# Kernel tuning notes

Measured on AMD Instinct MI355X. Metric: run time of the kernel, lower is better.

## Reference

```python
import jax, jax.numpy as jnp
import numpy as np

B = 4
C = 256
NUM_LEVELS = 5
REFINE_LEVEL = 2
NUM_POINTS = 9
GRAD_MUL = 0.1
SIZES = [160, 80, 40, 20, 10]


def conv2d(x, w, b=None, pad=0):
    out = jax.lax.conv_general_dilated(
        x, w, (1, 1), [(pad, pad), (pad, pad)],
        dimension_numbers=("NCHW", "OIHW", "NCHW"))
    if b is not None:
        out = out + b[None, :, None, None]
    return out


def nearest_resize(x, oh, ow):
    # torch F.interpolate(mode='nearest'): src index = floor(dst * in/out)
    H, W = x.shape[-2], x.shape[-1]
    iy = (jnp.arange(oh) * H) // oh
    ix = (jnp.arange(ow) * W) // ow
    return jnp.take(jnp.take(x, iy, axis=-2), ix, axis=-1)


def max_pool_to(x, oh, ow):
    # adaptive_max_pool2d with exactly-divisible sizes == strided max pool
    b, c, H, W = x.shape
    kh, kw = H // oh, W // ow
    return x.reshape(b, c, oh, kh, ow, kw).max(axis=(3, 5))


def deform_conv(x, offset, weight):
    # DeformConv v1 (mmcv), stride 1, pad 1, 3x3 kernel, no bias.
    # offset channels interleaved (dy, dx) per kernel point.
    b, c, H, W = x.shape
    K = weight.shape[-2] * weight.shape[-1]  # 9
    dy = offset[:, 0::2]  # (B,K,H,W)
    dx = offset[:, 1::2]
    base = jnp.arange(-1, 2, dtype=x.dtype)
    base_y = jnp.repeat(base, 3)  # (9,)
    base_x = jnp.tile(base, 3)
    py = jnp.arange(H, dtype=x.dtype)[None, None, :, None] + base_y[None, :, None, None] + dy
    px = jnp.arange(W, dtype=x.dtype)[None, None, None, :] + base_x[None, :, None, None] + dx
    y0 = jnp.floor(py)
    x0 = jnp.floor(px)
    xf = x.reshape(b, c, H * W)

    def gather(iy, ix):
        valid = ((iy >= 0) & (iy <= H - 1) & (ix >= 0) & (ix <= W - 1)).astype(x.dtype)
        flat = (jnp.clip(iy, 0, H - 1).astype(jnp.int32) * W
                + jnp.clip(ix, 0, W - 1).astype(jnp.int32)).reshape(b, -1)
        g = jax.vmap(lambda xb, ib: jnp.take(xb, ib, axis=1))(xf, flat)
        return g.reshape(b, c, K, H, W) * valid[:, None]

    wy1 = py - y0
    wx1 = px - x0
    wy0 = 1.0 - wy1
    wx0 = 1.0 - wx1
    val = (gather(y0, x0) * (wy0 * wx0)[:, None]
           + gather(y0, x0 + 1.0) * (wy0 * wx1)[:, None]
           + gather(y0 + 1.0, x0) * (wy1 * wx0)[:, None]
           + gather(y0 + 1.0, x0 + 1.0) * (wy1 * wx1)[:, None])  # (B,C,K,H,W)
    return jnp.einsum("bckhw,ock->bohw", val, weight.reshape(weight.shape[0], c, K))


def setup_inputs() -> dict:
    key = jax.random.key(0)
    ks = jax.random.split(key, 12)
    inp = {}
    for i, s in enumerate(SIZES):
        inp[f"x{i}"] = jax.random.normal(ks[i], (B, C, s, s), jnp.float32)
    inp["w_red1"] = jax.random.normal(ks[5], (NUM_LEVELS, 1, C, 3, 3), jnp.float32) * 0.02
    inp["b_red1"] = jnp.zeros((NUM_LEVELS, 1), jnp.float32)
    inp["w_red2"] = jax.random.normal(ks[6], (NUM_LEVELS, 1, C, 3, 3), jnp.float32) * 0.02
    inp["b_red2"] = jnp.zeros((NUM_LEVELS, 1), jnp.float32)
    inp["w_pts_conv"] = jax.random.normal(ks[7], (C, C, 3, 3), jnp.float32) * 0.02
    inp["b_pts_conv"] = jnp.zeros((C,), jnp.float32)
    inp["w_pts_out"] = jax.random.normal(ks[8], (2 * NUM_POINTS, C, 1, 1), jnp.float32) * 0.01
    inp["b_pts_out"] = jnp.zeros((2 * NUM_POINTS,), jnp.float32)
    inp["w_refine"] = jax.random.normal(ks[9], (C, C, 3, 3), jnp.float32) * 0.01
    return inp


def reference(x0, x1, x2, x3, x4, w_red1, b_red1, w_red2, b_red2,
              w_pts_conv, b_pts_conv, w_pts_out, b_pts_out, w_refine):
    inputs = [x0, x1, x2, x3, x4]
    gh, gw = inputs[REFINE_LEVEL].shape[-2], inputs[REFINE_LEVEL].shape[-1]
    feats = [max_pool_to(xi, gh, gw) if i < REFINE_LEVEL else nearest_resize(xi, gh, gw)
             for i, xi in enumerate(inputs)]
    ori_fe = sum(feats) / len(feats)

    pts = conv2d(jax.nn.relu(conv2d(ori_fe, w_pts_conv, b_pts_conv, pad=1)),
                 w_pts_out, b_pts_out, pad=0)
    pts_gm = (1.0 - GRAD_MUL) * jax.lax.stop_gradient(pts) + GRAD_MUL * pts

    base = jnp.arange(-1, 2, dtype=jnp.float32)
    base_off = jnp.stack([jnp.repeat(base, 3), jnp.tile(base, 3)], axis=1).reshape(-1)
    dcn_offset = pts_gm - base_off[None, :, None, None]

    bsf = jax.nn.relu(deform_conv(ori_fe, dcn_offset, w_refine))

    outs = []
    for i, xi in enumerate(inputs):
        h, w = xi.shape[-2], xi.shape[-1]
        # ConvModule default: conv -> (no norm) -> ReLU; then tanh per forward
        basic = jnp.tanh(jax.nn.relu(conv2d(xi, w_red1[i], b_red1[i], pad=1)))
        com = jnp.tanh(jax.nn.relu(conv2d(xi, w_red2[i], b_red2[i], pad=1)))
        att = nearest_resize(bsf, h, w) * (basic + com)
        outs.append(xi + att)
    return tuple(outs)
```

## Files before the change

kernel.cpp:

```cpp
#include <hip/hip_runtime.h>
#include <hip/hip_bf16.h>
#include <math.h>

constexpr int B_ = 4;
constexpr int C_ = 256;
constexpr int GH = 40, GW = 40, GP = 1600;
constexpr int KDIM = C_ * 9;
constexpr int MT = B_ * GP;

typedef __attribute__((ext_vector_type(8))) short short8b;
typedef __attribute__((ext_vector_type(4))) float f32x4;

__device__ inline ushort f2b(float f) {
    __hip_bfloat16 h = __float2bfloat16(f);
    return *reinterpret_cast<ushort*>(&h);
}
__device__ inline float b2f(ushort u) {
    unsigned v = (unsigned)u << 16;
    return *reinterpret_cast<float*>(&v);
}

__global__ __launch_bounds__(256) void fe_kernel(const float* __restrict__ x0,
                                                 const float* __restrict__ x1,
                                                 const float* __restrict__ x2,
                                                 const float* __restrict__ x3,
                                                 const float* __restrict__ x4,
                                                 float* __restrict__ fe_pm) {
    __shared__ float tile[64][65];
    int pix0 = blockIdx.x * 64;
    int c0 = blockIdx.y * 64;
    int b = blockIdx.z;
    int lx = threadIdx.x & 63;
    int ly = threadIdx.x >> 6;

    int pix = pix0 + lx;
    int h = pix / GW, w = pix - (pix / GW) * GW;
#pragma unroll
    for (int r = 0; r < 64; r += 4) {
        int c = c0 + ly + r;
        size_t bc = (size_t)b * C_ + c;
        const float* p0 = x0 + bc * 25600;
        float m0 = -INFINITY;
#pragma unroll
        for (int dy = 0; dy < 4; ++dy)
#pragma unroll
            for (int dx = 0; dx < 4; ++dx)
                m0 = fmaxf(m0, p0[(4 * h + dy) * 160 + 4 * w + dx]);
        const float* p1 = x1 + bc * 6400;
        float m1 = -INFINITY;
#pragma unroll
        for (int dy = 0; dy < 2; ++dy)
#pragma unroll
            for (int dx = 0; dx < 2; ++dx)
                m1 = fmaxf(m1, p1[(2 * h + dy) * 80 + 2 * w + dx]);
        float v2 = x2[bc * GP + pix];
        float v3 = x3[bc * 400 + (h / 2) * 20 + (w / 2)];
        float v4 = x4[bc * 100 + (h / 4) * 10 + (w / 4)];
        tile[ly + r][lx] = (m0 + m1 + v2 + v3 + v4) * 0.2f;
    }
    __syncthreads();
#pragma unroll
    for (int r = 0; r < 64; r += 4) {
        int p = ly + r;
        fe_pm[((size_t)b * GP + pix0 + p) * C_ + c0 + lx] = tile[lx][p];
    }
}

__global__ void wcvt_kernel(const float* __restrict__ wA, const float* __restrict__ wB,
                            ushort* __restrict__ oA, ushort* __restrict__ oB) {
    const float* w = blockIdx.y ? wB : wA;
    ushort* out = blockIdx.y ? oB : oA;
    int idx = blockIdx.x * 256 + threadIdx.x;
    int o = idx / KDIM;
    int rem = idx - o * KDIM;
    int c = rem / 9, t = rem - c * 9;
    out[(size_t)o * KDIM + t * 256 + c] = f2b(w[idx]);
}

__global__ void im2col_kernel(const float* __restrict__ fe_pm, ushort* __restrict__ A1) {
    int pix = blockIdx.x % GP, b = blockIdx.x / GP;
    int c = threadIdx.x;
    const float* fb = fe_pm + (size_t)b * GP * C_;
    ushort* dst = A1 + (size_t)blockIdx.x * KDIM;
    int h = pix / GW, w = pix - (pix / GW) * GW;
#pragma unroll
    for (int t = 0; t < 9; ++t) {
        int y = h + t / 3 - 1, x = w + t % 3 - 1;
        float v = (y >= 0 && y < GH && x >= 0 && x < GW) ? fb[(size_t)(y * GW + x) * C_ + c]
                                                         : 0.f;
        dst[t * 256 + c] = f2b(v);
    }
}

__global__ void sample_kernel(const float* __restrict__ fe_pm, const float* __restrict__ pts,
                              ushort* __restrict__ S) {
    int pix = blockIdx.x % GP, b = blockIdx.x / GP;
    int c = threadIdx.x;
    const float* fb = fe_pm + (size_t)b * GP * C_;
    const float* pb = pts + (size_t)b * 18 * GP + pix;
    ushort* dst = S + (size_t)blockIdx.x * KDIM;
    int h = pix / GW, w = pix - (pix / GW) * GW;
#pragma unroll
    for (int t = 0; t < 9; ++t) {
        float py = (float)h + pb[(2 * t) * GP];
        float px = (float)w + pb[(2 * t + 1) * GP];
        float y0f = floorf(py), x0f = floorf(px);
        int y0 = (int)y0f, x0 = (int)x0f;
        float wy1 = py - y0f, wx1 = px - x0f;
        float wy0 = 1.f - wy1, wx0 = 1.f - wx1;
        auto tap = [&](int yy, int xx) -> float {
            return (yy >= 0 && yy < GH && xx >= 0 && xx < GW)
                       ? fb[(size_t)(yy * GW + xx) * C_ + c]
                       : 0.f;
        };
        float v = tap(y0, x0) * wy0 * wx0 + tap(y0, x0 + 1) * wy0 * wx1 +
                  tap(y0 + 1, x0) * wy1 * wx0 + tap(y0 + 1, x0 + 1) * wy1 * wx1;
        dst[t * 256 + c] = f2b(v);
    }
}

__global__ __launch_bounds__(256) void mfma_gemm(const ushort* __restrict__ A,
                                                 const ushort* __restrict__ Bw,
                                                 const float* __restrict__ bias,
                                                 float* __restrict__ Cout) {
    __shared__ ushort As[2][64 * 64];
    __shared__ ushort Bs[2][64 * 64];
    int tid = threadIdx.x;
    int lane = tid & 63;
    int wid = tid >> 6;
    int wm = wid >> 1, wn = wid & 1;
    int m0 = blockIdx.x * 64;
    int n0 = blockIdx.y * 64;

    int sr = tid >> 3;
    int ss = tid & 7;
    int wsl = (ss ^ (sr & 7)) * 8;
    const ushort* gA0 = A + (size_t)(m0 + sr) * KDIM + ss * 8;
    const ushort* gA1 = A + (size_t)(m0 + sr + 32) * KDIM + ss * 8;
    const ushort* gB0 = Bw + (size_t)(n0 + sr) * KDIM + ss * 8;
    const ushort* gB1 = Bw + (size_t)(n0 + sr + 32) * KDIM + ss * 8;

    f32x4 acc[2][2];
#pragma unroll
    for (int i = 0; i < 2; ++i)
#pragma unroll
        for (int j = 0; j < 2; ++j) acc[i][j] = (f32x4){0.f, 0.f, 0.f, 0.f};

    short8b xA0, xA1, xB0, xB1;
    short8b yA0, yA1, yB0, yB1;

    auto loadX = [&]() {
        xA0 = *(const short8b*)gA0; xA1 = *(const short8b*)gA1;
        xB0 = *(const short8b*)gB0; xB1 = *(const short8b*)gB1;
        gA0 += 64; gA1 += 64; gB0 += 64; gB1 += 64;
    };
    auto loadY = [&]() {
        yA0 = *(const short8b*)gA0; yA1 = *(const short8b*)gA1;
        yB0 = *(const short8b*)gB0; yB1 = *(const short8b*)gB1;
        gA0 += 64; gA1 += 64; gB0 += 64; gB1 += 64;
    };
    auto writeL = [&](int buf, short8b a0, short8b a1, short8b b0, short8b b1) {
        *(short8b*)(As[buf] + sr * 64 + wsl) = a0;
        *(short8b*)(As[buf] + (sr + 32) * 64 + wsl) = a1;
        *(short8b*)(Bs[buf] + sr * 64 + wsl) = b0;
        *(short8b*)(Bs[buf] + (sr + 32) * 64 + wsl) = b1;
    };
    auto compute = [&](int cur) {
#pragma unroll
        for (int kq = 0; kq < 2; ++kq) {
            int k16 = kq * 4 + (lane >> 4);
            short8b af[2], bfr[2];
#pragma unroll
            for (int i = 0; i < 2; ++i) {
                int rA = wm * 32 + i * 16 + (lane & 15);
                af[i] = *(const short8b*)(As[cur] + rA * 64 + ((k16 ^ (rA & 7)) * 8));
                int rB = wn * 32 + i * 16 + (lane & 15);
                bfr[i] = *(const short8b*)(Bs[cur] + rB * 64 + ((k16 ^ (rB & 7)) * 8));
            }
#pragma unroll
            for (int in = 0; in < 2; ++in)
#pragma unroll
                for (int im = 0; im < 2; ++im)
                    acc[in][im] = __builtin_amdgcn_mfma_f32_16x16x32_bf16(
                        bfr[in], af[im], acc[in][im], 0, 0, 0);
        }
    };

    constexpr int NCH = KDIM / 64;
    loadX();
    loadY();
    writeL(0, xA0, xA1, xB0, xB1);
    __syncthreads();

    for (int kc = 0; kc < NCH; kc += 2) {
        if (kc + 2 < NCH) loadX();
        compute(0);
        writeL(1, yA0, yA1, yB0, yB1);
        __syncthreads();
        if (kc + 3 < NCH) loadY();
        compute(1);
        if (kc + 2 < NCH) writeL(0, xA0, xA1, xB0, xB1);
        __syncthreads();
    }

    int b = m0 / GP;
    int pix0 = m0 - b * GP;
    float* Cb = Cout + (size_t)b * C_ * GP;
#pragma unroll
    for (int in = 0; in < 2; ++in) {
#pragma unroll
        for (int r = 0; r < 4; ++r) {
            int n = n0 + wn * 32 + in * 16 + (lane >> 4) * 4 + r;
            float bv = bias ? bias[n] : 0.f;
#pragma unroll
            for (int im = 0; im < 2; ++im) {
                int m = pix0 + wm * 32 + im * 16 + (lane & 15);
                Cb[(size_t)n * GP + m] = fmaxf(acc[in][im][r] + bv, 0.f);
            }
        }
    }
}

__global__ void pts_kernel(const float* __restrict__ p1, const float* __restrict__ wpo,
                           const float* __restrict__ bpo, float* __restrict__ pts) {
    int idx = blockIdx.x * 256 + threadIdx.x;
    int pix = idx % GP;
    int p = (idx / GP) % 18;
    int b = idx / (GP * 18);
    const float* pb = p1 + (size_t)b * C_ * GP + pix;
    const float* wp = wpo + p * C_;
    float s = bpo[p];
    for (int c = 0; c < C_; ++c) s += pb[(size_t)c * GP] * wp[c];
    pts[idx] = s;
}

__device__ constexpr int L_S[5] = {160, 80, 40, 20, 10};
__device__ constexpr int L_NPX[5] = {102400, 25600, 6400, 1600, 400};
__device__ constexpr int YK_START[5] = {0, 400, 500, 525, 532};
__device__ constexpr int FC_START[5] = {0, 1600, 2000, 2100, 2125};
__device__ constexpr size_t L_YBASE[5] = {0, 7372800, 9216000, 9676800, 9792000};
__device__ constexpr size_t L_OUT[5] = {0, 26214400, 32768000, 34406400, 34816000};

__device__ inline int lvl_of(int bx, const int* start) {
    return (bx >= start[4]) ? 4 : (bx >= start[3]) ? 3 : (bx >= start[2]) ? 2
           : (bx >= start[1]) ? 1 : 0;
}

__global__ __launch_bounds__(256) void yk_all(const float* __restrict__ x0,
                                              const float* __restrict__ x1,
                                              const float* __restrict__ x2,
                                              const float* __restrict__ x3,
                                              const float* __restrict__ x4,
                                              const float* __restrict__ w_red1,
                                              const float* __restrict__ w_red2,
                                              ushort* __restrict__ y_all) {
    int bx = blockIdx.x;
    int lvl = lvl_of(bx, YK_START);
    const float* x = lvl == 0 ? x0 : lvl == 1 ? x1 : lvl == 2 ? x2 : lvl == 3 ? x3 : x4;
    int s = L_S[lvl];
    int npx = L_NPX[lvl];
    int bp = (bx - YK_START[lvl]) * 256 + threadIdx.x;
    int g = blockIdx.y;
    if (bp >= npx) return;
    int ss_ = s * s;
    int b = bp / ss_;
    int p = bp - b * ss_;
    const float* xg = x + ((size_t)b * C_ + g * 64) * ss_ + p;
    const float* w1g = w_red1 + (size_t)lvl * KDIM + g * 64 * 9;
    const float* w2g = w_red2 + (size_t)lvl * KDIM + g * 64 * 9;
    float a1[9] = {}, a2[9] = {};
#pragma unroll 4
    for (int ci = 0; ci < 64; ++ci) {
        float v = xg[(size_t)ci * ss_];
#pragma unroll
        for (int t = 0; t < 9; ++t) {
            a1[t] += w1g[ci * 9 + t] * v;
            a2[t] += w2g[ci * 9 + t] * v;
        }
    }
    ushort* yb = y_all + L_YBASE[lvl] + bp;
#pragma unroll
    for (int t = 0; t < 9; ++t) {
        yb[(size_t)(g * 18 + t) * npx] = f2b(a1[t]);
        yb[(size_t)(g * 18 + 9 + t) * npx] = f2b(a2[t]);
    }
}

__global__ __launch_bounds__(256) void fincomb_all(const float* __restrict__ x0,
                                                   const float* __restrict__ x1,
                                                   const float* __restrict__ x2,
                                                   const float* __restrict__ x3,
                                                   const float* __restrict__ x4,
                                                   const ushort* __restrict__ y_all,
                                                   const float* __restrict__ b_red1,
                                                   const float* __restrict__ b_red2,
                                                   const float* __restrict__ bsf,
                                                   float* __restrict__ out) {
    __shared__ float red[2][4][64];
    __shared__ float amap_s[64];
    int bx = blockIdx.x;
    int lvl = lvl_of(bx, FC_START);
    const float* x = lvl == 0 ? x0 : lvl == 1 ? x1 : lvl == 2 ? x2 : lvl == 3 ? x3 : x4;
    int s = L_S[lvl];
    int npx = L_NPX[lvl];
    const ushort* y = y_all + L_YBASE[lvl];
    float* out_l = out + L_OUT[lvl];
    int lane = threadIdx.x & 63;
    int grp = threadIdx.x >> 6;
    int pix_g = (bx - FC_START[lvl]) * 64 + lane;
    bool valid = pix_g < npx;
    int pg = valid ? pix_g : 0;
    int ss_ = s * s;
    int b = pg / ss_;
    int pix = pg - b * ss_;
    int h = pix / s, w = pix - h * s;
    const ushort* yg = y + (size_t)grp * 18 * npx;
    float s1 = 0.f, s2 = 0.f;
#pragma unroll
    for (int t = 0; t < 9; ++t) {
        int dy = t / 3 - 1, dx = t % 3 - 1;
        int hy = h + dy, wx = w + dx;
        if (hy >= 0 && hy < s && wx >= 0 && wx < s) {
            int qq = pg + dy * s + dx;
            s1 += b2f(yg[(size_t)t * npx + qq]);
            s2 += b2f(yg[(size_t)(9 + t) * npx + qq]);
        }
    }
    red[0][grp][lane] = s1;
    red[1][grp][lane] = s2;
    __syncthreads();
    if (grp == 0) {
        float t1 = red[0][0][lane] + red[0][1][lane] + red[0][2][lane] + red[0][3][lane];
        float t2 = red[1][0][lane] + red[1][1][lane] + red[1][2][lane] + red[1][3][lane];
        t1 = tanhf(fmaxf(t1 + b_red1[lvl], 0.f));
        t2 = tanhf(fmaxf(t2 + b_red2[lvl], 0.f));
        amap_s[lane] = t1 + t2;
    }
    __syncthreads();
    if (!valid) return;
    float av = amap_s[lane];
    int gh = h * GH / s, gw = w * GW / s;
    const float* bb = bsf + (size_t)b * C_ * GP + gh * GW + gw;
    const float* xp = x + ((size_t)b * C_ + grp * 64) * ss_ + pix;
    float* op = out_l + ((size_t)b * C_ + grp * 64) * ss_ + pix;
#pragma unroll 4
    for (int ci = 0; ci < 64; ++ci) {
        int c = grp * 64 + ci;
        op[(size_t)ci * ss_] = xp[(size_t)ci * ss_] + bb[(size_t)c * GP] * av;
    }
}

extern "C" void kernel_launch(void* const* d_in, const int* in_sizes, int n_in,
                              void* d_out, int out_size, void* d_ws, size_t ws_size,
                              hipStream_t stream) {
    const float* x[5];
    for (int i = 0; i < 5; ++i) x[i] = (const float*)d_in[i];
    const float* w_red1 = (const float*)d_in[5];
    const float* b_red1 = (const float*)d_in[6];
    const float* w_red2 = (const float*)d_in[7];
    const float* b_red2 = (const float*)d_in[8];
    const float* w_pts_conv = (const float*)d_in[9];
    const float* b_pts_conv = (const float*)d_in[10];
    const float* w_pts_out = (const float*)d_in[11];
    const float* b_pts_out = (const float*)d_in[12];
    const float* w_refine = (const float*)d_in[13];
    float* out = (float*)d_out;

    float* ws = (float*)d_ws;
    float* fe_pm = ws;
    float* p1 = fe_pm + 1638400;
    float* pts = p1 + 1638400;
    float* bsf = pts + 115200;
    ushort* y_all = (ushort*)(bsf + 1638400);
    ushort* AS_buf = y_all + 9820800;
    ushort* Wb1 = AS_buf + (size_t)MT * KDIM;
    ushort* Wb2 = Wb1 + (size_t)C_ * KDIM;

    fe_kernel<<<dim3(25, 4, B_), 256, 0, stream>>>(x[0], x[1], x[2], x[3], x[4], fe_pm);
    wcvt_kernel<<<dim3(2304, 2), 256, 0, stream>>>(w_pts_conv, w_refine, Wb1, Wb2);
    im2col_kernel<<<MT, 256, 0, stream>>>(fe_pm, AS_buf);
    mfma_gemm<<<dim3(100, 4), 256, 0, stream>>>(AS_buf, Wb1, b_pts_conv, p1);
    pts_kernel<<<450, 256, 0, stream>>>(p1, w_pts_out, b_pts_out, pts);
    sample_kernel<<<MT, 256, 0, stream>>>(fe_pm, pts, AS_buf);
    mfma_gemm<<<dim3(100, 4), 256, 0, stream>>>(AS_buf, Wb2, nullptr, bsf);
    yk_all<<<dim3(534, 4), 256, 0, stream>>>(x[0], x[1], x[2], x[3], x[4],
                                             w_red1, w_red2, y_all);
    fincomb_all<<<2132, 256, 0, stream>>>(x[0], x[1], x[2], x[3], x[4], y_all,
                                          b_red1, b_red2, bsf, out);
}
```

Measured before the change: 228.2 us.

## Fuse im2col into implicit-GEMM conv and store pooled features as bf16

Removes the explicit im2col kernel by having the GEMM load A tiles directly from the pixel-major bf16 feature map with per-tap pixel shifts and a validity mask. The pooled feature map is now stored in bf16, which halves its footprint for the sample kernel and the GEMM. The GEMM M-tile shrinks from 64 to 32 rows, doubling the grid to 800 blocks for better CU occupancy, at the cost of less B-tile reuse per block. The padded workspace lets shifted loads stay in bounds, and rows that fall outside the image are zeroed in registers.

```diff
diff --git a/kernel.cpp b/kernel.cpp
--- a/kernel.cpp
+++ b/kernel.cpp
@@ -7,6 +7,7 @@
 constexpr int GH = 40, GW = 40, GP = 1600;
 constexpr int KDIM = C_ * 9;
 constexpr int MT = B_ * GP;
+constexpr int FPAD = 64;
 
 typedef __attribute__((ext_vector_type(8))) short short8b;
 typedef __attribute__((ext_vector_type(4))) float f32x4;
@@ -25,7 +26,7 @@
                                                  const float* __restrict__ x2,
                                                  const float* __restrict__ x3,
                                                  const float* __restrict__ x4,
-                                                 float* __restrict__ fe_pm) {
+                                                 ushort* __restrict__ feb) {
     __shared__ float tile[64][65];
     int pix0 = blockIdx.x * 64;
     int c0 = blockIdx.y * 64;
@@ -62,7 +63,7 @@
 #pragma unroll
     for (int r = 0; r < 64; r += 4) {
         int p = ly + r;
-        fe_pm[((size_t)b * GP + pix0 + p) * C_ + c0 + lx] = tile[lx][p];
+        feb[((size_t)b * GP + pix0 + p) * C_ + c0 + lx] = f2b(tile[lx][p]);
     }
 }
 
@@ -77,26 +78,11 @@
     out[(size_t)o * KDIM + t * 256 + c] = f2b(w[idx]);
 }
 
-__global__ void im2col_kernel(const float* __restrict__ fe_pm, ushort* __restrict__ A1) {
-    int pix = blockIdx.x % GP, b = blockIdx.x / GP;
-    int c = threadIdx.x;
-    const float* fb = fe_pm + (size_t)b * GP * C_;
-    ushort* dst = A1 + (size_t)blockIdx.x * KDIM;
-    int h = pix / GW, w = pix - (pix / GW) * GW;
-#pragma unroll
-    for (int t = 0; t < 9; ++t) {
-        int y = h + t / 3 - 1, x = w + t % 3 - 1;
-        float v = (y >= 0 && y < GH && x >= 0 && x < GW) ? fb[(size_t)(y * GW + x) * C_ + c]
-                                                         : 0.f;
-        dst[t * 256 + c] = f2b(v);
-    }
-}
-
-__global__ void sample_kernel(const float* __restrict__ fe_pm, const float* __restrict__ pts,
+__global__ void sample_kernel(const ushort* __restrict__ feb, const float* __restrict__ pts,
                               ushort* __restrict__ S) {
     int pix = blockIdx.x % GP, b = blockIdx.x / GP;
     int c = threadIdx.x;
-    const float* fb = fe_pm + (size_t)b * GP * C_;
+    const ushort* fb = feb + (size_t)b * GP * C_;
     const float* pb = pts + (size_t)b * 18 * GP + pix;
     ushort* dst = S + (size_t)blockIdx.x * KDIM;
     int h = pix / GW, w = pix - (pix / GW) * GW;
@@ -110,7 +96,7 @@
         float wy0 = 1.f - wy1, wx0 = 1.f - wx1;
         auto tap = [&](int yy, int xx) -> float {
             return (yy >= 0 && yy < GH && xx >= 0 && xx < GW)
-                       ? fb[(size_t)(yy * GW + xx) * C_ + c]
+                       ? b2f(fb[(size_t)(yy * GW + xx) * C_ + c])
                        : 0.f;
         };
         float v = tap(y0, x0) * wy0 * wx0 + tap(y0, x0 + 1) * wy0 * wx1 +
@@ -119,104 +105,111 @@
     }
 }
 
+template <int IMPLICIT>
 __global__ __launch_bounds__(256) void mfma_gemm(const ushort* __restrict__ A,
                                                  const ushort* __restrict__ Bw,
                                                  const float* __restrict__ bias,
                                                  float* __restrict__ Cout) {
-    __shared__ ushort As[2][64 * 64];
+    __shared__ ushort As[2][32 * 64];
     __shared__ ushort Bs[2][64 * 64];
     int tid = threadIdx.x;
     int lane = tid & 63;
     int wid = tid >> 6;
     int wm = wid >> 1, wn = wid & 1;
-    int m0 = blockIdx.x * 64;
+    int m0 = blockIdx.x * 32;
     int n0 = blockIdx.y * 64;
 
     int sr = tid >> 3;
     int ss = tid & 7;
     int wsl = (ss ^ (sr & 7)) * 8;
-    const ushort* gA0 = A + (size_t)(m0 + sr) * KDIM + ss * 8;
-    const ushort* gA1 = A + (size_t)(m0 + sr + 32) * KDIM + ss * 8;
-    const ushort* gB0 = Bw + (size_t)(n0 + sr) * KDIM + ss * 8;
-    const ushort* gB1 = Bw + (size_t)(n0 + sr + 32) * KDIM + ss * 8;
-
-    f32x4 acc[2][2];
-#pragma unroll
-    for (int i = 0; i < 2; ++i)
-#pragma unroll
-        for (int j = 0; j < 2; ++j) acc[i][j] = (f32x4){0.f, 0.f, 0.f, 0.f};
-
-    short8b xA0, xA1, xB0, xB1;
-    short8b yA0, yA1, yB0, yB1;
-
-    auto loadX = [&]() {
-        xA0 = *(const short8b*)gA0; xA1 = *(const short8b*)gA1;
-        xB0 = *(const short8b*)gB0; xB1 = *(const short8b*)gB1;
-        gA0 += 64; gA1 += 64; gB0 += 64; gB1 += 64;
+
+    int b = m0 / GP;
+    int pix0 = m0 - b * GP;
+    int my_pix = pix0 + wm * 16 + (lane & 15);
+    int mh = my_pix / GW, mw = my_pix - (my_pix / GW) * GW;
+    int vmask = 0;
+#pragma unroll
+    for (int t = 0; t < 9; ++t) {
+        int dy = t / 3 - 1, dx = t % 3 - 1;
+        if (mh + dy >= 0 && mh + dy < GH && mw + dx >= 0 && mw + dx < GW)
+            vmask |= 1 << t;
+    }
+    static __device__ const int DSH[9] = {-GW - 1, -GW, -GW + 1, -1, 0, 1, GW - 1, GW, GW + 1};
+
+    f32x4 acc[2];
+    acc[0] = (f32x4){0.f, 0.f, 0.f, 0.f};
+    acc[1] = (f32x4){0.f, 0.f, 0.f, 0.f};
+
+    short8b xA, xB0, xB1;
+    short8b yA, yB0, yB1;
+
+    auto loadA = [&](int kc) -> short8b {
+        if (IMPLICIT) {
+            int t = kc >> 2;
+            int c0 = (kc & 3) * 64;
+            const ushort* p = A + (long)(m0 + DSH[t] + sr) * C_ + c0 + ss * 8;
+            return *(const short8b*)p;
+        } else {
+            const ushort* p = A + (size_t)(m0 + sr) * KDIM + kc * 64 + ss * 8;
+            return *(const short8b*)p;
+        }
     };
-    auto loadY = [&]() {
-        yA0 = *(const short8b*)gA0; yA1 = *(const short8b*)gA1;
-        yB0 = *(const short8b*)gB0; yB1 = *(const short8b*)gB1;
-        gA0 += 64; gA1 += 64; gB0 += 64; gB1 += 64;
+    auto loadB = [&](int kc, short8b& b0, short8b& b1) {
+        const ushort* src = Bw + (size_t)(n0 + sr) * KDIM + kc * 64 + ss * 8;
+        b0 = *(const short8b*)src;
+        b1 = *(const short8b*)(src + (size_t)32 * KDIM);
     };
-    auto writeL = [&](int buf, short8b a0, short8b a1, short8b b0, short8b b1) {
-        *(short8b*)(As[buf] + sr * 64 + wsl) = a0;
-        *(short8b*)(As[buf] + (sr + 32) * 64 + wsl) = a1;
+    auto writeL = [&](int buf, short8b a, short8b b0, short8b b1) {
+        *(short8b*)(As[buf] + sr * 64 + wsl) = a;
         *(short8b*)(Bs[buf] + sr * 64 + wsl) = b0;
         *(short8b*)(Bs[buf] + (sr + 32) * 64 + wsl) = b1;
     };
-    auto compute = [&](int cur) {
+    auto compute = [&](int cur, int t) {
+        bool vt = !IMPLICIT || ((vmask >> t) & 1);
 #pragma unroll
         for (int kq = 0; kq < 2; ++kq) {
             int k16 = kq * 4 + (lane >> 4);
-            short8b af[2], bfr[2];
+            int rA = wm * 16 + (lane & 15);
+            short8b af = *(const short8b*)(As[cur] + rA * 64 + ((k16 ^ (rA & 7)) * 8));
+            if (IMPLICIT && !vt) af = short8b{0, 0, 0, 0, 0, 0, 0, 0};
+            short8b bfr[2];
 #pragma unroll
             for (int i = 0; i < 2; ++i) {
-                int rA = wm * 32 + i * 16 + (lane & 15);
-                af[i] = *(const short8b*)(As[cur] + rA * 64 + ((k16 ^ (rA & 7)) * 8));
                 int rB = wn * 32 + i * 16 + (lane & 15);
                 bfr[i] = *(const short8b*)(Bs[cur] + rB * 64 + ((k16 ^ (rB & 7)) * 8));
             }
 #pragma unroll
             for (int in = 0; in < 2; ++in)
-#pragma unroll
-                for (int im = 0; im < 2; ++im)
-                    acc[in][im] = __builtin_amdgcn_mfma_f32_16x16x32_bf16(
-                        bfr[in], af[im], acc[in][im], 0, 0, 0);
+                acc[in] = __builtin_amdgcn_mfma_f32_16x16x32_bf16(bfr[in], af, acc[in], 0, 0, 0);
         }
     };
 
     constexpr int NCH = KDIM / 64;
-    loadX();
-    loadY();
-    writeL(0, xA0, xA1, xB0, xB1);
+    xA = loadA(0); loadB(0, xB0, xB1);
+    yA = loadA(1); loadB(1, yB0, yB1);
+    writeL(0, xA, xB0, xB1);
     __syncthreads();
 
     for (int kc = 0; kc < NCH; kc += 2) {
-        if (kc + 2 < NCH) loadX();
-        compute(0);
-        writeL(1, yA0, yA1, yB0, yB1);
+        if (kc + 2 < NCH) { xA = loadA(kc + 2); loadB(kc + 2, xB0, xB1); }
+        compute(0, kc >> 2);
+        writeL(1, yA, yB0, yB1);
         __syncthreads();
-        if (kc + 3 < NCH) loadY();
-        compute(1);
-        if (kc + 2 < NCH) writeL(0, xA0, xA1, xB0, xB1);
+        if (kc + 3 < NCH) { yA = loadA(kc + 3); loadB(kc + 3, yB0, yB1); }
+        compute(1, (kc + 1) >> 2);
+        if (kc + 2 < NCH) writeL(0, xA, xB0, xB1);
         __syncthreads();
     }
 
-    int b = m0 / GP;
-    int pix0 = m0 - b * GP;
     float* Cb = Cout + (size_t)b * C_ * GP;
+    int m = pix0 + wm * 16 + (lane & 15);
 #pragma unroll
     for (int in = 0; in < 2; ++in) {
 #pragma unroll
         for (int r = 0; r < 4; ++r) {
             int n = n0 + wn * 32 + in * 16 + (lane >> 4) * 4 + r;
             float bv = bias ? bias[n] : 0.f;
-#pragma unroll
-            for (int im = 0; im < 2; ++im) {
-                int m = pix0 + wm * 32 + im * 16 + (lane & 15);
-                Cb[(size_t)n * GP + m] = fmaxf(acc[in][im][r] + bv, 0.f);
-            }
+            Cb[(size_t)n * GP + m] = fmaxf(acc[in][r] + bv, 0.f);
         }
     }
 }
@@ -366,9 +359,9 @@
     const float* w_refine = (const float*)d_in[13];
     float* out = (float*)d_out;
 
-    float* ws = (float*)d_ws;
-    float* fe_pm = ws;
-    float* p1 = fe_pm + 1638400;
+    ushort* feb_base = (ushort*)d_ws;
+    ushort* feb = feb_base + (size_t)FPAD * C_;
+    float* p1 = (float*)(feb_base + (size_t)(MT + 2 * FPAD) * C_);
     float* pts = p1 + 1638400;
     float* bsf = pts + 115200;
     ushort* y_all = (ushort*)(bsf + 1638400);
@@ -376,13 +369,12 @@
     ushort* Wb1 = AS_buf + (size_t)MT * KDIM;
     ushort* Wb2 = Wb1 + (size_t)C_ * KDIM;
 
-    fe_kernel<<<dim3(25, 4, B_), 256, 0, stream>>>(x[0], x[1], x[2], x[3], x[4], fe_pm);
+    fe_kernel<<<dim3(25, 4, B_), 256, 0, stream>>>(x[0], x[1], x[2], x[3], x[4], feb);
     wcvt_kernel<<<dim3(2304, 2), 256, 0, stream>>>(w_pts_conv, w_refine, Wb1, Wb2);
-    im2col_kernel<<<MT, 256, 0, stream>>>(fe_pm, AS_buf);
-    mfma_gemm<<<dim3(100, 4), 256, 0, stream>>>(AS_buf, Wb1, b_pts_conv, p1);
+    mfma_gemm<1><<<dim3(200, 4), 256, 0, stream>>>(feb, Wb1, b_pts_conv, p1);
     pts_kernel<<<450, 256, 0, stream>>>(p1, w_pts_out, b_pts_out, pts);
-    sample_kernel<<<MT, 256, 0, stream>>>(fe_pm, pts, AS_buf);
-    mfma_gemm<<<dim3(100, 4), 256, 0, stream>>>(AS_buf, Wb2, nullptr, bsf);
+    sample_kernel<<<MT, 256, 0, stream>>>(feb, pts, AS_buf);
+    mfma_gemm<0><<<dim3(200, 4), 256, 0, stream>>>(AS_buf, Wb2, nullptr, bsf);
     yk_all<<<dim3(534, 4), 256, 0, stream>>>(x[0], x[1], x[2], x[3], x[4],
                                              w_red1, w_red2, y_all);
     fincomb_all<<<2132, 256, 0, stream>>>(x[0], x[1], x[2], x[3], x[4], y_all,
```

Measured after the change: 241.2 us. 1.06x slower.

## Split-K the two bf16 MFMA GEMMs three ways with separate reduce kernel

Applied to the files above, without the earlier changes.

The two 6400x256x2304 GEMMs are split along K into three slices launched as a z-dimension, which triples the block count from 400 to 1200 so the GPU's compute units are better filled. Each slice writes fp32 partials to a new workspace buffer. A separate reduce kernel then sums the three partials and applies bias and ReLU. This trades extra global traffic (about 20 MB of partials written and read per GEMM) and two extra launches for higher occupancy.

```diff
diff --git a/kernel.cpp b/kernel.cpp
--- a/kernel.cpp
+++ b/kernel.cpp
@@ -6,7 +6,9 @@
 constexpr int C_ = 256;
 constexpr int GH = 40, GW = 40, GP = 1600;
 constexpr int KDIM = C_ * 9;
+constexpr int KSPL = 768;
 constexpr int MT = B_ * GP;
+constexpr int NELEM = B_ * C_ * GP;
 
 typedef __attribute__((ext_vector_type(8))) short short8b;
 typedef __attribute__((ext_vector_type(4))) float f32x4;
@@ -121,8 +123,7 @@
 
 __global__ __launch_bounds__(256) void mfma_gemm(const ushort* __restrict__ A,
                                                  const ushort* __restrict__ Bw,
-                                                 const float* __restrict__ bias,
-                                                 float* __restrict__ Cout) {
+                                                 float* __restrict__ Cpart) {
     __shared__ ushort As[2][64 * 64];
     __shared__ ushort Bs[2][64 * 64];
     int tid = threadIdx.x;
@@ -131,14 +132,15 @@
     int wm = wid >> 1, wn = wid & 1;
     int m0 = blockIdx.x * 64;
     int n0 = blockIdx.y * 64;
+    int zs = blockIdx.z;
 
     int sr = tid >> 3;
     int ss = tid & 7;
     int wsl = (ss ^ (sr & 7)) * 8;
-    const ushort* gA0 = A + (size_t)(m0 + sr) * KDIM + ss * 8;
-    const ushort* gA1 = A + (size_t)(m0 + sr + 32) * KDIM + ss * 8;
-    const ushort* gB0 = Bw + (size_t)(n0 + sr) * KDIM + ss * 8;
-    const ushort* gB1 = Bw + (size_t)(n0 + sr + 32) * KDIM + ss * 8;
+    const ushort* gA0 = A + (size_t)(m0 + sr) * KDIM + zs * KSPL + ss * 8;
+    const ushort* gA1 = A + (size_t)(m0 + sr + 32) * KDIM + zs * KSPL + ss * 8;
+    const ushort* gB0 = Bw + (size_t)(n0 + sr) * KDIM + zs * KSPL + ss * 8;
+    const ushort* gB1 = Bw + (size_t)(n0 + sr + 32) * KDIM + zs * KSPL + ss * 8;
 
     f32x4 acc[2][2];
 #pragma unroll
@@ -186,7 +188,7 @@
         }
     };
 
-    constexpr int NCH = KDIM / 64;
+    constexpr int NCH = KSPL / 64;
     loadX();
     loadY();
     writeL(0, xA0, xA1, xB0, xB1);
@@ -205,20 +207,28 @@
 
     int b = m0 / GP;
     int pix0 = m0 - b * GP;
-    float* Cb = Cout + (size_t)b * C_ * GP;
+    float* Cb = Cpart + (size_t)zs * NELEM + (size_t)b * C_ * GP;
 #pragma unroll
     for (int in = 0; in < 2; ++in) {
 #pragma unroll
         for (int r = 0; r < 4; ++r) {
             int n = n0 + wn * 32 + in * 16 + (lane >> 4) * 4 + r;
-            float bv = bias ? bias[n] : 0.f;
 #pragma unroll
             for (int im = 0; im < 2; ++im) {
                 int m = pix0 + wm * 32 + im * 16 + (lane & 15);
-                Cb[(size_t)n * GP + m] = fmaxf(acc[in][im][r] + bv, 0.f);
+                Cb[(size_t)n * GP + m] = acc[in][im][r];
             }
         }
     }
+}
+
+__global__ __launch_bounds__(256) void reduce3_kernel(const float* __restrict__ parts,
+                                                      const float* __restrict__ bias,
+                                                      float* __restrict__ dst) {
+    int idx = blockIdx.x * 256 + threadIdx.x;
+    float v = parts[idx] + parts[idx + NELEM] + parts[idx + 2 * NELEM];
+    if (bias) v += bias[(idx / GP) & 255];
+    dst[idx] = fmaxf(v, 0.f);
 }
 
 __global__ void pts_kernel(const float* __restrict__ p1, const float* __restrict__ wpo,
@@ -371,7 +381,8 @@
     float* p1 = fe_pm + 1638400;
     float* pts = p1 + 1638400;
     float* bsf = pts + 115200;
-    ushort* y_all = (ushort*)(bsf + 1638400);
+    float* parts = bsf + 1638400;
+    ushort* y_all = (ushort*)(parts + 4915200);
     ushort* AS_buf = y_all + 9820800;
     ushort* Wb1 = AS_buf + (size_t)MT * KDIM;
     ushort* Wb2 = Wb1 + (size_t)C_ * KDIM;
@@ -379,10 +390,12 @@
     fe_kernel<<<dim3(25, 4, B_), 256, 0, stream>>>(x[0], x[1], x[2], x[3], x[4], fe_pm);
     wcvt_kernel<<<dim3(2304, 2), 256, 0, stream>>>(w_pts_conv, w_refine, Wb1, Wb2);
     im2col_kernel<<<MT, 256, 0, stream>>>(fe_pm, AS_buf);
-    mfma_gemm<<<dim3(100, 4), 256, 0, stream>>>(AS_buf, Wb1, b_pts_conv, p1);
+    mfma_gemm<<<dim3(100, 4, 3), 256, 0, stream>>>(AS_buf, Wb1, parts);
+    reduce3_kernel<<<6400, 256, 0, stream>>>(parts, b_pts_conv, p1);
     pts_kernel<<<450, 256, 0, stream>>>(p1, w_pts_out, b_pts_out, pts);
     sample_kernel<<<MT, 256, 0, stream>>>(fe_pm, pts, AS_buf);
-    mfma_gemm<<<dim3(100, 4), 256, 0, stream>>>(AS_buf, Wb2, nullptr, bsf);
+    mfma_gemm<<<dim3(100, 4, 3), 256, 0, stream>>>(AS_buf, Wb2, parts);
+    reduce3_kernel<<<6400, 256, 0, stream>>>(parts, nullptr, bsf);
     yk_all<<<dim3(534, 4), 256, 0, stream>>>(x[0], x[1], x[2], x[3], x[4],
                                              w_red1, w_red2, y_all);
     fincomb_all<<<2132, 256, 0, stream>>>(x[0], x[1], x[2], x[3], x[4], y_all,
```

New measurement: 247.7 us. +8.6%, slower.

## Co-schedule reduction-conv blocks inside the two MFMA GEMM launches

Applied to the files above, without the earlier changes.

Merges the yk reduction-conv work into the two GEMM kernels as extra blocks. Each GEMM launch carries 400 GEMM tiles plus 1068 yk blocks covering two of the four channel groups. The GEMM grid is flattened to 1D. The aim is to fill the GPU while the small GEMM grid (400 blocks) underuses the CUs, and to remove one launch. The risk is that yk blocks take on the GEMM kernel's LDS allocation and register budget, which may lower occupancy for them.

```diff
diff --git a/kernel.cpp b/kernel.cpp
--- a/kernel.cpp
+++ b/kernel.cpp
@@ -7,6 +7,7 @@
 constexpr int GH = 40, GW = 40, GP = 1600;
 constexpr int KDIM = C_ * 9;
 constexpr int MT = B_ * GP;
+constexpr int NGEMM = 400;
 
 typedef __attribute__((ext_vector_type(8))) short short8b;
 typedef __attribute__((ext_vector_type(4))) float f32x4;
@@ -119,18 +120,81 @@
     }
 }
 
-__global__ __launch_bounds__(256) void mfma_gemm(const ushort* __restrict__ A,
-                                                 const ushort* __restrict__ Bw,
-                                                 const float* __restrict__ bias,
-                                                 float* __restrict__ Cout) {
+__device__ constexpr int L_S[5] = {160, 80, 40, 20, 10};
+__device__ constexpr int L_NPX[5] = {102400, 25600, 6400, 1600, 400};
+__device__ constexpr int YK_START[5] = {0, 400, 500, 525, 532};
+__device__ constexpr int FC_START[5] = {0, 1600, 2000, 2100, 2125};
+__device__ constexpr size_t L_YBASE[5] = {0, 7372800, 9216000, 9676800, 9792000};
+__device__ constexpr size_t L_OUT[5] = {0, 26214400, 32768000, 34406400, 34816000};
+
+__device__ inline int lvl_of(int bx, const int* start) {
+    return (bx >= start[4]) ? 4 : (bx >= start[3]) ? 3 : (bx >= start[2]) ? 2
+           : (bx >= start[1]) ? 1 : 0;
+}
+
+__device__ inline void yk_body(int bx, int g, const float* x0, const float* x1,
+                               const float* x2, const float* x3, const float* x4,
+                               const float* w_red1, const float* w_red2,
+                               ushort* y_all) {
+    int lvl = lvl_of(bx, YK_START);
+    const float* x = lvl == 0 ? x0 : lvl == 1 ? x1 : lvl == 2 ? x2 : lvl == 3 ? x3 : x4;
+    int s = L_S[lvl];
+    int npx = L_NPX[lvl];
+    int bp = (bx - YK_START[lvl]) * 256 + threadIdx.x;
+    if (bp >= npx) return;
+    int ss_ = s * s;
+    int b = bp / ss_;
+    int p = bp - b * ss_;
+    const float* xg = x + ((size_t)b * C_ + g * 64) * ss_ + p;
+    const float* w1g = w_red1 + (size_t)lvl * KDIM + g * 64 * 9;
+    const float* w2g = w_red2 + (size_t)lvl * KDIM + g * 64 * 9;
+    float a1[9] = {}, a2[9] = {};
+#pragma unroll 4
+    for (int ci = 0; ci < 64; ++ci) {
+        float v = xg[(size_t)ci * ss_];
+#pragma unroll
+        for (int t = 0; t < 9; ++t) {
+            a1[t] += w1g[ci * 9 + t] * v;
+            a2[t] += w2g[ci * 9 + t] * v;
+        }
+    }
+    ushort* yb = y_all + L_YBASE[lvl] + bp;
+#pragma unroll
+    for (int t = 0; t < 9; ++t) {
+        yb[(size_t)(g * 18 + t) * npx] = f2b(a1[t]);
+        yb[(size_t)(g * 18 + 9 + t) * npx] = f2b(a2[t]);
+    }
+}
+
+__global__ __launch_bounds__(256) void gemm_yk(const ushort* __restrict__ A,
+                                               const ushort* __restrict__ Bw,
+                                               const float* __restrict__ bias,
+                                               float* __restrict__ Cout,
+                                               const float* __restrict__ x0,
+                                               const float* __restrict__ x1,
+                                               const float* __restrict__ x2,
+                                               const float* __restrict__ x3,
+                                               const float* __restrict__ x4,
+                                               const float* __restrict__ w_red1,
+                                               const float* __restrict__ w_red2,
+                                               ushort* __restrict__ y_all,
+                                               int g_base) {
     __shared__ ushort As[2][64 * 64];
     __shared__ ushort Bs[2][64 * 64];
+
+    if (blockIdx.x >= NGEMM) {
+        int bxx = blockIdx.x - NGEMM;
+        int g = g_base + bxx / 534;
+        yk_body(bxx % 534, g, x0, x1, x2, x3, x4, w_red1, w_red2, y_all);
+        return;
+    }
+
     int tid = threadIdx.x;
     int lane = tid & 63;
     int wid = tid >> 6;
     int wm = wid >> 1, wn = wid & 1;
-    int m0 = blockIdx.x * 64;
-    int n0 = blockIdx.y * 64;
+    int m0 = (blockIdx.x >> 2) * 64;
+    int n0 = (blockIdx.x & 3) * 64;
 
     int sr = tid >> 3;
     int ss = tid & 7;
@@ -232,58 +296,6 @@
     float s = bpo[p];
     for (int c = 0; c < C_; ++c) s += pb[(size_t)c * GP] * wp[c];
     pts[idx] = s;
-}
-
-__device__ constexpr int L_S[5] = {160, 80, 40, 20, 10};
-__device__ constexpr int L_NPX[5] = {102400, 25600, 6400, 1600, 400};
-__device__ constexpr int YK_START[5] = {0, 400, 500, 525, 532};
-__device__ constexpr int FC_START[5] = {0, 1600, 2000, 2100, 2125};
-__device__ constexpr size_t L_YBASE[5] = {0, 7372800, 9216000, 9676800, 9792000};
-__device__ constexpr size_t L_OUT[5] = {0, 26214400, 32768000, 34406400, 34816000};
-
-__device__ inline int lvl_of(int bx, const int* start) {
-    return (bx >= start[4]) ? 4 : (bx >= start[3]) ? 3 : (bx >= start[2]) ? 2
-           : (bx >= start[1]) ? 1 : 0;
-}
-
-__global__ __launch_bounds__(256) void yk_all(const float* __restrict__ x0,
-                                              const float* __restrict__ x1,
-                                              const float* __restrict__ x2,
-                                              const float* __restrict__ x3,
-                                              const float* __restrict__ x4,
-                                              const float* __restrict__ w_red1,
-                                              const float* __restrict__ w_red2,
-                                              ushort* __restrict__ y_all) {
-    int bx = blockIdx.x;
-    int lvl = lvl_of(bx, YK_START);
-    const float* x = lvl == 0 ? x0 : lvl == 1 ? x1 : lvl == 2 ? x2 : lvl == 3 ? x3 : x4;
-    int s = L_S[lvl];
-    int npx = L_NPX[lvl];
-    int bp = (bx - YK_START[lvl]) * 256 + threadIdx.x;
-    int g = blockIdx.y;
-    if (bp >= npx) return;
-    int ss_ = s * s;
-    int b = bp / ss_;
-    int p = bp - b * ss_;
-    const float* xg = x + ((size_t)b * C_ + g * 64) * ss_ + p;
-    const float* w1g = w_red1 + (size_t)lvl * KDIM + g * 64 * 9;
-    const float* w2g = w_red2 + (size_t)lvl * KDIM + g * 64 * 9;
-    float a1[9] = {}, a2[9] = {};
-#pragma unroll 4
-    for (int ci = 0; ci < 64; ++ci) {
-        float v = xg[(size_t)ci * ss_];
-#pragma unroll
-        for (int t = 0; t < 9; ++t) {
-            a1[t] += w1g[ci * 9 + t] * v;
-            a2[t] += w2g[ci * 9 + t] * v;
-        }
-    }
-    ushort* yb = y_all + L_YBASE[lvl] + bp;
-#pragma unroll
-    for (int t = 0; t < 9; ++t) {
-        yb[(size_t)(g * 18 + t) * npx] = f2b(a1[t]);
-        yb[(size_t)(g * 18 + 9 + t) * npx] = f2b(a2[t]);
-    }
 }
 
 __global__ __launch_bounds__(256) void fincomb_all(const float* __restrict__ x0,
@@ -379,12 +391,14 @@
     fe_kernel<<<dim3(25, 4, B_), 256, 0, stream>>>(x[0], x[1], x[2], x[3], x[4], fe_pm);
     wcvt_kernel<<<dim3(2304, 2), 256, 0, stream>>>(w_pts_conv, w_refine, Wb1, Wb2);
     im2col_kernel<<<MT, 256, 0, stream>>>(fe_pm, AS_buf);
-    mfma_gemm<<<dim3(100, 4), 256, 0, stream>>>(AS_buf, Wb1, b_pts_conv, p1);
+    gemm_yk<<<NGEMM + 1068, 256, 0, stream>>>(AS_buf, Wb1, b_pts_conv, p1,
+                                              x[0], x[1], x[2], x[3], x[4],
+                                              w_red1, w_red2, y_all, 0);
     pts_kernel<<<450, 256, 0, stream>>>(p1, w_pts_out, b_pts_out, pts);
     sample_kernel<<<MT, 256, 0, stream>>>(fe_pm, pts, AS_buf);
-    mfma_gemm<<<dim3(100, 4), 256, 0, stream>>>(AS_buf, Wb2, nullptr, bsf);
-    yk_all<<<dim3(534, 4), 256, 0, stream>>>(x[0], x[1], x[2], x[3], x[4],
-                                             w_red1, w_red2, y_all);
+    gemm_yk<<<NGEMM + 1068, 256, 0, stream>>>(AS_buf, Wb2, nullptr, bsf,
+                                              x[0], x[1], x[2], x[3], x[4],
+                                              w_red1, w_red2, y_all, 2);
     fincomb_all<<<2132, 256, 0, stream>>>(x[0], x[1], x[2], x[3], x[4], y_all,
                                           b_red1, b_red2, bsf, out);
 }
```

New measurement: 237.8 us. 4.2% more time.
